# Kernel tuning notes

Hardware: AMD Instinct MI355X
Metric: run time of the kernel (lower is better)

The kernel has to match this reference:

```python
import jax, jax.numpy as jnp
import numpy as np

TOP_K = 2
NEG_INF = -1.0e9


def setup_inputs() -> dict:
    key = jax.random.key(0)
    k = jax.random.split(key, 5)
    B, S, D, E = 4, 2048, 1024, 8
    H = 2 * D
    x = jax.random.normal(k[0], (B, S, D), dtype=jnp.float32)
    gate_w = jax.random.normal(k[1], (D, E), dtype=jnp.float32) * 0.02
    gate_b = jnp.zeros((E,), dtype=jnp.float32)
    w1 = jax.random.normal(k[2], (E, D, H), dtype=jnp.float32) * 0.02
    b1 = jnp.zeros((E, H), dtype=jnp.float32)
    w2 = jax.random.normal(k[3], (E, H, D), dtype=jnp.float32) * 0.02
    b2 = jnp.zeros((E, D), dtype=jnp.float32)
    noise = jax.random.normal(k[4], (B, S, E), dtype=jnp.float32)
    return {"x": x, "gate_w": gate_w, "gate_b": gate_b,
            "w1": w1, "b1": b1, "w2": w2, "b2": b2, "noise": noise}


def reference(x, gate_w, gate_b, w1, b1, w2, b2, noise):
    B, S, D = x.shape
    # Gating: linear + small gaussian noise (hk.next_rng_key equivalent)
    gating_logits = jnp.einsum('bsd,de->bse', x, gate_w) + gate_b + noise * 0.01
    # keep_top_k: mask all but top-k logits to -1e9
    top_k_values, top_k_indices = jax.lax.top_k(gating_logits, TOP_K)
    mask = gating_logits >= jnp.min(top_k_values, axis=-1, keepdims=True)
    gating_logits = jnp.where(mask, gating_logits, NEG_INF)
    gating_probs = jax.nn.softmax(gating_logits, axis=-1)
    # Dense compute of ALL experts on ALL tokens (as in source): [E,B,S,D]
    h = jax.nn.silu(jnp.einsum('bsd,edh->ebsh', x, w1) + b1[:, None, None, :])
    expert_outputs = jnp.einsum('ebsh,ehd->ebsd', h, w2) + b2[:, None, None, :]
    # Gather top-k expert outputs per token: [B,S,K,D]
    bi = jnp.arange(B)[:, None, None]
    si = jnp.arange(S)[None, :, None]
    selected = expert_outputs[top_k_indices, bi, si]
    top_k_gating_probs = jnp.take_along_axis(gating_probs, top_k_indices, axis=-1)
    final_output = jnp.einsum('bskd,bsk->bsd', selected, top_k_gating_probs)
    # Load-balancing aux loss on the MASKED logits (as in source)
    routing_probs = jax.nn.softmax(gating_logits, axis=-1)
    expert_usage = jnp.sum(routing_probs, axis=(0, 1))
    expert_importance = expert_usage / jnp.sum(expert_usage)
    mean_imp = jnp.mean(expert_importance)
    std_imp = jnp.std(expert_importance)
    aux_loss = std_imp / (mean_imp + 1e-10)
    return final_output, top_k_indices, aux_loss
```

## Files before the change

### kernel.cpp

```cpp
#include <hip/hip_runtime.h>
#include <stdint.h>


#define NTOK   8192
#define DIM    1024
#define NEXP   8
#define HID    2048
#define OUT_MAIN (NTOK * DIM)
#define IDX_OFF  OUT_MAIN
#define AUX_OFF  (OUT_MAIN + NTOK * 2)
#define MAXBLK 72

typedef __attribute__((ext_vector_type(8))) short short8;
typedef __attribute__((ext_vector_type(4))) float floatx4;

__device__ __forceinline__ unsigned short f2bf(float f) {
  unsigned int b = __float_as_uint(f);
  b += 0x7FFFu + ((b >> 16) & 1u);
  return (unsigned short)(b >> 16);
}

__global__ __launch_bounds__(1024) void k_gating(
    const float* __restrict__ x, const float* __restrict__ gate_w,
    const float* __restrict__ gate_b, const float* __restrict__ noise,
    float* __restrict__ out, int* __restrict__ counts,
    int* __restrict__ lists_tok, float* __restrict__ lists_p,
    float* __restrict__ probs_all, unsigned short* __restrict__ xb)
{
  const int lane = threadIdx.x & 63;
  const int wv   = threadIdx.x >> 6;
  const int t    = blockIdx.x * 16 + wv;
  const float* xr = x + (size_t)t * DIM;

  __shared__ int   cnt[NEXP];
  __shared__ int   base[NEXP];
  __shared__ int   s_e[32];
  __shared__ int   s_pos[32];
  __shared__ float s_p[32];
  if (threadIdx.x < NEXP) cnt[threadIdx.x] = 0;

  double acc[NEXP] = {0,0,0,0,0,0,0,0};
  #pragma unroll
  for (int jj = 0; jj < 4; ++jj) {
    const int d0 = lane * 4 + jj * 256;
    const float4 xv = *(const float4*)(xr + d0);
    const float xs[4] = {xv.x, xv.y, xv.z, xv.w};
    unsigned short xbq[4];
    #pragma unroll
    for (int c = 0; c < 4; ++c) {
      const float4 g0 = *(const float4*)(gate_w + (size_t)(d0 + c) * NEXP);
      const float4 g1 = *(const float4*)(gate_w + (size_t)(d0 + c) * NEXP + 4);
      const double xd = (double)xs[c];
      acc[0] += xd * (double)g0.x; acc[1] += xd * (double)g0.y;
      acc[2] += xd * (double)g0.z; acc[3] += xd * (double)g0.w;
      acc[4] += xd * (double)g1.x; acc[5] += xd * (double)g1.y;
      acc[6] += xd * (double)g1.z; acc[7] += xd * (double)g1.w;
      xbq[c] = f2bf(xs[c]);
    }
    ushort4 q; q.x = xbq[0]; q.y = xbq[1]; q.z = xbq[2]; q.w = xbq[3];
    *(ushort4*)(xb + (size_t)t * DIM + d0) = q;
  }
  #pragma unroll
  for (int e = 0; e < NEXP; ++e) {
    #pragma unroll
    for (int off = 32; off; off >>= 1) acc[e] += __shfl_xor(acc[e], off);
  }
  __syncthreads();
  if (lane == 0) {
    double l[NEXP];
    #pragma unroll
    for (int e = 0; e < NEXP; ++e)
      l[e] = acc[e] + (double)gate_b[e] + 0.01 * (double)noise[(size_t)t * NEXP + e];
    int i1 = 0; double v1 = l[0];
    #pragma unroll
    for (int e = 1; e < NEXP; ++e) if (l[e] > v1) { v1 = l[e]; i1 = e; }
    int i2 = (i1 == 0) ? 1 : 0; double v2 = l[i2];
    #pragma unroll
    for (int e = 0; e < NEXP; ++e) if (e != i1 && l[e] > v2) { v2 = l[e]; i2 = e; }
    float pr[NEXP]; float Z = 0.f;
    #pragma unroll
    for (int e = 0; e < NEXP; ++e) {
      const float a = (l[e] >= v2) ? (float)(l[e] - v1) : -1.0e9f;
      pr[e] = __expf(a); Z += pr[e];
    }
    const float rz = 1.0f / Z;
    #pragma unroll
    for (int e = 0; e < NEXP; ++e) {
      pr[e] *= rz;
      probs_all[(size_t)t * NEXP + e] = pr[e];
    }
    out[(size_t)IDX_OFF + t * 2]     = (float)i1;
    out[(size_t)IDX_OFF + t * 2 + 1] = (float)i2;
    const int p1 = atomicAdd(&cnt[i1], 1);
    const int p2 = atomicAdd(&cnt[i2], 1);
    s_e[wv * 2]     = i1; s_pos[wv * 2]     = p1; s_p[wv * 2]     = pr[i1];
    s_e[wv * 2 + 1] = i2; s_pos[wv * 2 + 1] = p2; s_p[wv * 2 + 1] = pr[i2];
  }
  __syncthreads();
  if (threadIdx.x < NEXP) base[threadIdx.x] = atomicAdd(&counts[threadIdx.x], cnt[threadIdx.x]);
  __syncthreads();
  if (lane == 0) {
    #pragma unroll
    for (int k = 0; k < 2; ++k) {
      const int ee  = s_e[wv * 2 + k];
      const int pos = base[ee] + s_pos[wv * 2 + k];
      lists_tok[ee * NTOK + pos] = t;
      lists_p[ee * NTOK + pos]   = s_p[wv * 2 + k];
    }
  }
}

__global__ void k_offs(const int* __restrict__ counts, int* __restrict__ offs,
                       int* __restrict__ tbl_e, int* __restrict__ tbl_m,
                       int* __restrict__ nblk) {
  if (threadIdx.x == 0) {
    int a = 0;
    #pragma unroll
    for (int e = 0; e < NEXP; ++e) { offs[e] = a; a += counts[e]; }
    offs[NEXP] = a;
    int ent_e[MAXBLK], ent_m[MAXBLK];
    int nb = 0;
    for (int e = 0; e < NEXP; ++e) {
      const int nbe = (counts[e] + 255) >> 8;
      for (int m = 0; m < nbe; ++m) { ent_e[nb] = e; ent_m[nb] = m << 8; ++nb; }
    }
    nblk[0] = nb;
    for (int p = 0; p < MAXBLK; ++p) { tbl_e[p] = -1; tbl_m[p] = 0; }
    const int q = nb >> 3, r = nb & 7;
    for (int c = 0; c < 8; ++c) {
      const int cnt   = q + (c < r ? 1 : 0);
      const int start = c * q + (c < r ? c : r);
      for (int t = 0; t < cnt; ++t) {
        const int pos = c + (t << 3);
        tbl_e[pos] = ent_e[start + t];
        tbl_m[pos] = ent_m[start + t];
      }
    }
  }
}

__global__ __launch_bounds__(256) void k_aux(const float* __restrict__ probs_all,
                                             float* __restrict__ out) {
  float p[NEXP] = {0,0,0,0,0,0,0,0};
  for (int t = threadIdx.x; t < NTOK; t += 256) {
    const float4 a = *(const float4*)(probs_all + (size_t)t * NEXP);
    const float4 b = *(const float4*)(probs_all + (size_t)t * NEXP + 4);
    p[0] += a.x; p[1] += a.y; p[2] += a.z; p[3] += a.w;
    p[4] += b.x; p[5] += b.y; p[6] += b.z; p[7] += b.w;
  }
  #pragma unroll
  for (int e = 0; e < NEXP; ++e) {
    #pragma unroll
    for (int off = 32; off; off >>= 1) p[e] += __shfl_xor(p[e], off);
  }
  __shared__ float red[4][NEXP];
  const int lane = threadIdx.x & 63, wv = threadIdx.x >> 6;
  if (lane == 0) {
    #pragma unroll
    for (int e = 0; e < NEXP; ++e) red[wv][e] = p[e];
  }
  __syncthreads();
  if (threadIdx.x == 0) {
    float usage[NEXP], s = 0.f;
    #pragma unroll
    for (int e = 0; e < NEXP; ++e) {
      usage[e] = red[0][e] + red[1][e] + red[2][e] + red[3][e];
      s += usage[e];
    }
    float imp[NEXP], mean = 0.f, var = 0.f;
    #pragma unroll
    for (int e = 0; e < NEXP; ++e) { imp[e] = usage[e] / s; mean += imp[e]; }
    mean *= 0.125f;
    #pragma unroll
    for (int e = 0; e < NEXP; ++e) { const float d = imp[e] - mean; var += d * d; }
    var *= 0.125f;
    out[AUX_OFF] = sqrtf(var) / (mean + 1e-10f);
  }
}

__global__ __launch_bounds__(256) void k_tr(
    const float* __restrict__ in, unsigned short* __restrict__ out,
    int in_ld, size_t in_estride, int r0, int c0,
    int out_ld, size_t out_estride)
{
  const int e  = blockIdx.z;
  const int tr = blockIdx.x << 6;
  const int tc = blockIdx.y << 6;
  const int tid = threadIdx.x;
  __shared__ float t[64][65];
  const float* src = in + (size_t)e * in_estride + (size_t)(r0 + tr) * in_ld + (c0 + tc);
  #pragma unroll
  for (int p = 0; p < 4; ++p) {
    const int r  = (p << 4) + (tid >> 4);
    const int c4 = (tid & 15) << 2;
    const float4 v = *(const float4*)(src + (size_t)r * in_ld + c4);
    t[r][c4] = v.x; t[r][c4 + 1] = v.y; t[r][c4 + 2] = v.z; t[r][c4 + 3] = v.w;
  }
  __syncthreads();
  unsigned short* dst = out + (size_t)e * out_estride + (size_t)tc * out_ld + tr;
  #pragma unroll
  for (int p = 0; p < 4; ++p) {
    const int c  = (p << 4) + (tid >> 4);
    const int r4 = (tid & 15) << 2;
    ushort4 q;
    q.x = f2bf(t[r4][c]);     q.y = f2bf(t[r4 + 1][c]);
    q.z = f2bf(t[r4 + 2][c]); q.w = f2bf(t[r4 + 3][c]);
    *(ushort4*)(dst + (size_t)c * out_ld + r4) = q;
  }
}

template <int MODE>
__global__ __launch_bounds__(512, 2) void k_gemm(
    const unsigned short* __restrict__ Abase,
    const unsigned short* __restrict__ Bt,
    const float* __restrict__ bias,
    const int* __restrict__ counts, const int* __restrict__ offs,
    const int* __restrict__ tbl_e, const int* __restrict__ tbl_m,
    const int* __restrict__ nblk,
    const int* __restrict__ lists_tok, const float* __restrict__ lists_p,
    unsigned short* __restrict__ hout, float* __restrict__ out,
    const int hb, const int Hs)
{
  const int bx = blockIdx.x;
  const int e  = tbl_e[bx];
  if (e < 0) return;
  const int m0  = tbl_m[bx];
  const int n_e = counts[e];
  const int nb  = blockIdx.y << 8;

  const int Kloc = (MODE == 0) ? DIM : Hs;
  const int nt   = Kloc >> 6;

  const int tid  = threadIdx.x;
  const int lane = tid & 63;
  const int wv   = tid >> 6;
  const int wm   = (wv & 1) << 7;
  const int wn   = (wv >> 1) << 6;

  __shared__ __align__(16) unsigned short as[2][256 * 64];
  __shared__ __align__(16) unsigned short bs[2][256 * 64];
  unsigned short* const A0 = &as[0][0]; unsigned short* const A1 = &as[1][0];
  unsigned short* const B0 = &bs[0][0]; unsigned short* const B1 = &bs[1][0];

  const unsigned short* Bexp = Bt + (size_t)e * ((size_t)DIM * Hs) + (size_t)nb * Kloc;

  const int off_sh = ((lane & 7) ^ (lane >> 3)) << 3;
  const int r0  = (wv << 3) + (lane >> 3);
  const int rb0 = ((wv >> 2) << 6) + ((wv & 3) << 3) + (lane >> 3);
  const unsigned short* pA0; const unsigned short* pA1;
  const unsigned short* pA2; const unsigned short* pA3;
  {
    const unsigned short* p[4];
    #pragma unroll
    for (int qq = 0; qq < 4; ++qq) {
      const int rr = m0 + r0 + (qq << 6);
      const int rc = (rr < n_e) ? rr : (n_e - 1);
      size_t arow;
      if (MODE == 0) arow = (size_t)lists_tok[e * NTOK + rc] * DIM;
      else           arow = (size_t)(offs[e] + rc) * Hs;
      p[qq] = Abase + arow + off_sh;
    }
    pA0 = p[0]; pA1 = p[1]; pA2 = p[2]; pA3 = p[3];
  }
  const unsigned short* pB0 = Bexp + (size_t)rb0 * Kloc + off_sh;
  const unsigned short* pB1 = Bexp + (size_t)(rb0 + 32) * Kloc + off_sh;
  const unsigned short* pB2 = Bexp + (size_t)(rb0 + 128) * Kloc + off_sh;
  const unsigned short* pB3 = Bexp + (size_t)(rb0 + 160) * Kloc + off_sh;
  const int dA = (wv << 3) * 64;
  const int dB = (((wv >> 2) << 6) + ((wv & 3) << 3)) * 64;

  auto ST = [&](const unsigned short* g, unsigned short* l) {
    __builtin_amdgcn_global_load_lds(
        (const __attribute__((address_space(1))) void*)g,
        (__attribute__((address_space(3))) void*)(void*)l, 16, 0, 0);
  };
  auto STG_A0 = [&](unsigned short* ab, int t) { if (t < nt) { const int kk = t << 6;
      ST(pA0 + kk, ab + dA); ST(pA2 + kk, ab + 2 * 4096 + dA); } };
  auto STG_A1 = [&](unsigned short* ab, int t) { if (t < nt) { const int kk = t << 6;
      ST(pA1 + kk, ab + 4096 + dA); ST(pA3 + kk, ab + 3 * 4096 + dA); } };
  auto STG_B0 = [&](unsigned short* bb, int t) { if (t < nt) { const int kk = t << 6;
      ST(pB0 + kk, bb + dB); ST(pB2 + kk, bb + 8192 + dB); } };
  auto STG_B1 = [&](unsigned short* bb, int t) { if (t < nt) { const int kk = t << 6;
      ST(pB1 + kk, bb + 2048 + dB); ST(pB3 + kk, bb + 10240 + dB); } };

  auto LDA8 = [&](const unsigned short* ab, int i, int s) -> short8 {
    const int row = wm + (i << 4) + (lane & 15);
    const int ck  = (((s << 2) | (lane >> 4)) ^ (row & 7)) << 3;
    return *(const short8*)(ab + row * 64 + ck);
  };
  auto LDB8 = [&](const unsigned short* bb, int j, int s) -> short8 {
    const int row = wn + (j << 4) + (lane & 15);
    const int ck  = (((s << 2) | (lane >> 4)) ^ (row & 7)) << 3;
    return *(const short8*)(bb + row * 64 + ck);
  };

  floatx4 acc[8][4];
  #pragma unroll
  for (int i = 0; i < 8; ++i)
    #pragma unroll
    for (int j = 0; j < 4; ++j) acc[i][j] = (floatx4){0.f, 0.f, 0.f, 0.f};

  STG_A0(A0, 0); STG_B1(B0, 0); STG_A1(A0, 0); STG_B0(B0, 0);
  STG_A0(A1, 1); STG_B1(B1, 1); STG_A1(A1, 1);

  short8 a_[4][2], b_[2][2];
  for (int u = 0; u < nt; ++u) {
    const int p = u & 1;
    const unsigned short* ap = p ? A1 : A0;
    const unsigned short* bp = p ? B1 : B0;
    unsigned short* apn = p ? A0 : A1;
    unsigned short* apc = p ? A1 : A0;
    unsigned short* bpn = p ? B0 : B1;
    unsigned short* bpc = p ? B1 : B0;
    (void)apn;

    STG_B0(bpn, u + 1);
    if (u + 1 < nt) { asm volatile("s_waitcnt vmcnt(8)" ::: "memory"); }
    else            { asm volatile("s_waitcnt vmcnt(0)" ::: "memory"); }
    __builtin_amdgcn_sched_barrier(0);
    __builtin_amdgcn_s_barrier();
    __builtin_amdgcn_sched_barrier(0);
    #pragma unroll
    for (int i = 0; i < 4; ++i) { a_[i][0] = LDA8(ap, i, 0); a_[i][1] = LDA8(ap, i, 1); }
    #pragma unroll
    for (int j = 0; j < 2; ++j) { b_[j][0] = LDB8(bp, j, 0); b_[j][1] = LDB8(bp, j, 1); }
    asm volatile("s_waitcnt lgkmcnt(0)" ::: "memory");
    __builtin_amdgcn_sched_barrier(0);
    __builtin_amdgcn_s_setprio(1);
    #pragma unroll
    for (int s = 0; s < 2; ++s)
      #pragma unroll
      for (int i = 0; i < 4; ++i)
        #pragma unroll
        for (int j = 0; j < 2; ++j)
          acc[i][j] = __builtin_amdgcn_mfma_f32_16x16x32_bf16(a_[i][s], b_[j][s], acc[i][j], 0, 0, 0);
    __builtin_amdgcn_s_setprio(0);
    __builtin_amdgcn_sched_barrier(0);
    __builtin_amdgcn_s_barrier();
    __builtin_amdgcn_sched_barrier(0);

    STG_A0(apc, u + 2);
    #pragma unroll
    for (int j = 0; j < 2; ++j) { b_[j][0] = LDB8(bp, j + 2, 0); b_[j][1] = LDB8(bp, j + 2, 1); }
    __builtin_amdgcn_sched_barrier(0);
    __builtin_amdgcn_s_barrier();
    __builtin_amdgcn_sched_barrier(0);
    asm volatile("s_waitcnt lgkmcnt(0)" ::: "memory");
    __builtin_amdgcn_sched_barrier(0);
    __builtin_amdgcn_s_setprio(1);
    #pragma unroll
    for (int s = 0; s < 2; ++s)
      #pragma unroll
      for (int i = 0; i < 4; ++i)
        #pragma unroll
        for (int j = 0; j < 2; ++j)
          acc[i][j + 2] = __builtin_amdgcn_mfma_f32_16x16x32_bf16(a_[i][s], b_[j][s], acc[i][j + 2], 0, 0, 0);
    __builtin_amdgcn_s_setprio(0);
    __builtin_amdgcn_sched_barrier(0);
    __builtin_amdgcn_s_barrier();
    __builtin_amdgcn_sched_barrier(0);

    STG_B1(bpc, u + 2);
    #pragma unroll
    for (int i = 0; i < 4; ++i) { a_[i][0] = LDA8(ap, i + 4, 0); a_[i][1] = LDA8(ap, i + 4, 1); }
    __builtin_amdgcn_sched_barrier(0);
    __builtin_amdgcn_s_barrier();
    __builtin_amdgcn_sched_barrier(0);
    asm volatile("s_waitcnt lgkmcnt(0)" ::: "memory");
    __builtin_amdgcn_sched_barrier(0);
    __builtin_amdgcn_s_setprio(1);
    #pragma unroll
    for (int s = 0; s < 2; ++s)
      #pragma unroll
      for (int i = 0; i < 4; ++i)
        #pragma unroll
        for (int j = 0; j < 2; ++j)
          acc[i + 4][j + 2] = __builtin_amdgcn_mfma_f32_16x16x32_bf16(a_[i][s], b_[j][s], acc[i + 4][j + 2], 0, 0, 0);
    __builtin_amdgcn_s_setprio(0);
    __builtin_amdgcn_sched_barrier(0);
    __builtin_amdgcn_s_barrier();
    __builtin_amdgcn_sched_barrier(0);

    STG_A1(apc, u + 2);
    #pragma unroll
    for (int j = 0; j < 2; ++j) { b_[j][0] = LDB8(bp, j, 0); b_[j][1] = LDB8(bp, j, 1); }
    __builtin_amdgcn_sched_barrier(0);
    __builtin_amdgcn_s_barrier();
    __builtin_amdgcn_sched_barrier(0);
    asm volatile("s_waitcnt lgkmcnt(0)" ::: "memory");
    __builtin_amdgcn_sched_barrier(0);
    __builtin_amdgcn_s_setprio(1);
    #pragma unroll
    for (int s = 0; s < 2; ++s)
      #pragma unroll
      for (int i = 0; i < 4; ++i)
        #pragma unroll
        for (int j = 0; j < 2; ++j)
          acc[i + 4][j] = __builtin_amdgcn_mfma_f32_16x16x32_bf16(a_[i][s], b_[j][s], acc[i + 4][j], 0, 0, 0);
    __builtin_amdgcn_s_setprio(0);
    __builtin_amdgcn_sched_barrier(0);
    __builtin_amdgcn_s_barrier();
    __builtin_amdgcn_sched_barrier(0);
  }

  const int q4 = (lane >> 4) << 2;
  if (MODE == 0) {
    #pragma unroll
    for (int i = 0; i < 8; ++i) {
      #pragma unroll
      for (int j = 0; j < 4; ++j) {
        const int nloc = wn + (j << 4) + (lane & 15);
        const float bb = bias[e * HID + hb + nb + nloc];
        #pragma unroll
        for (int rr = 0; rr < 4; ++rr) {
          const int m = m0 + wm + (i << 4) + q4 + rr;
          if (m < n_e) {
            float v = acc[i][j][rr] + bb;
            v = v / (1.0f + __expf(-v));
            hout[(size_t)(offs[e] + m) * Hs + nb + nloc] = f2bf(v);
          }
        }
      }
    }
  } else {
    #pragma unroll
    for (int i = 0; i < 8; ++i) {
      #pragma unroll
      for (int rr = 0; rr < 4; ++rr) {
        const int m = m0 + wm + (i << 4) + q4 + rr;
        if (m < n_e) {
          const int   tok = lists_tok[e * NTOK + m];
          const float pp  = lists_p[e * NTOK + m];
          #pragma unroll
          for (int j = 0; j < 4; ++j) {
            const int d = nb + wn + (j << 4) + (lane & 15);
            float v = acc[i][j][rr];
            if (hb == 0) v += bias[e * DIM + d];
            atomicAdd(out + (size_t)tok * DIM + d, pp * v);
          }
        }
      }
    }
  }
}

extern "C" void kernel_launch(void* const* d_in, const int* in_sizes, int n_in,
                              void* d_out, int out_size, void* d_ws, size_t ws_size,
                              hipStream_t stream)
{
  const float* x      = (const float*)d_in[0];
  const float* gate_w = (const float*)d_in[1];
  const float* gate_b = (const float*)d_in[2];
  const float* w1     = (const float*)d_in[3];
  const float* b1     = (const float*)d_in[4];
  const float* w2     = (const float*)d_in[5];
  const float* b2     = (const float*)d_in[6];
  const float* noise  = (const float*)d_in[7];
  float* out = (float*)d_out;

  char* ws = (char*)d_ws;
  const size_t CNT_OFF = 0;
  const size_t OFF_OFF = 64;
  const size_t NBK_OFF = 128;
  const size_t TBE_OFF = 192;
  const size_t TBM_OFF = 1024;
  const size_t LT_OFF  = 2048;
  const size_t LP_OFF  = LT_OFF + 262144;
  const size_t PA_OFF  = LP_OFF + 262144;
  const size_t XB_OFF  = 1048576;
  const size_t W_OFF   = 17825792;

  int nsl = 0;
  for (int cand = 1; cand <= 8; cand <<= 1) {
    const size_t need = W_OFF + (size_t)(33554432 + 67108864) / (size_t)cand;
    if (ws_size >= need) { nsl = cand; break; }
  }
  if (!nsl) return;
  const int Hs = HID / nsl;

  int* counts          = (int*)(ws + CNT_OFF);
  int* offs            = (int*)(ws + OFF_OFF);
  int* nblk            = (int*)(ws + NBK_OFF);
  int* tbl_e           = (int*)(ws + TBE_OFF);
  int* tbl_m           = (int*)(ws + TBM_OFF);
  int* lists_tok       = (int*)(ws + LT_OFF);
  float* lists_p       = (float*)(ws + LP_OFF);
  float* probs_all     = (float*)(ws + PA_OFF);
  unsigned short* xb   = (unsigned short*)(ws + XB_OFF);
  unsigned short* wt   = (unsigned short*)(ws + W_OFF);
  unsigned short* hbuf = (unsigned short*)(ws + W_OFF + (size_t)33554432 / nsl);

  hipMemsetAsync(d_out, 0, (size_t)OUT_MAIN * sizeof(float), stream);
  hipMemsetAsync(ws + CNT_OFF, 0, 64, stream);

  k_gating<<<NTOK / 16, 1024, 0, stream>>>(x, gate_w, gate_b, noise, out, counts,
                                           lists_tok, lists_p, probs_all, xb);
  k_offs<<<1, 64, 0, stream>>>(counts, offs, tbl_e, tbl_m, nblk);
  k_aux<<<1, 256, 0, stream>>>(probs_all, out);

  for (int s = 0; s < nsl; ++s) {
    const int hb = s * Hs;
    dim3 gt1(DIM / 64, Hs / 64, NEXP);
    k_tr<<<gt1, 256, 0, stream>>>(w1, wt, HID, (size_t)DIM * HID, 0, hb,
                                  DIM, (size_t)Hs * DIM);
    dim3 g1(MAXBLK, Hs / 256, 1);
    k_gemm<0><<<g1, 512, 0, stream>>>(xb, wt, b1, counts, offs, tbl_e, tbl_m, nblk,
                                      lists_tok, lists_p, hbuf, out, hb, Hs);
    dim3 gt2(Hs / 64, DIM / 64, NEXP);
    k_tr<<<gt2, 256, 0, stream>>>(w2, wt, DIM, (size_t)DIM * HID, hb, 0,
                                  Hs, (size_t)DIM * Hs);
    dim3 g2(MAXBLK, DIM / 256, 1);
    k_gemm<1><<<g2, 512, 0, stream>>>(hbuf, wt, b2, counts, offs, tbl_e, tbl_m, nblk,
                                      lists_tok, lists_p, hbuf, out, hb, Hs);
  }
}
```

Measured before the change: 496.4 us.

## Split-K the second expert GEMM and reorder the MFMA pipeline stages

The down-projection GEMM gets a split-K over two halves of the hidden dimension, which doubles its grid so more CUs are occupied, and the partial sums are combined through the atomicAdd epilogue that already exists. The bias is added only by the first K-half. The main loop is also reorganised: A fragments are reused across B halves in a different quadrant order, the explicit lgkmcnt waits between phases are removed, and the vmcnt threshold changes. In exchange the output gets twice as many atomic adds, and dropping the LDS waits leans on the compiler to insert them correctly.

```diff
diff --git a/kernel.cpp b/kernel.cpp
--- a/kernel.cpp
+++ b/kernel.cpp
@@ -226,10 +226,12 @@
   if (e < 0) return;
   const int m0  = tbl_m[bx];
   const int n_e = counts[e];
-  const int nb  = blockIdx.y << 8;
-
-  const int Kloc = (MODE == 0) ? DIM : Hs;
-  const int nt   = Kloc >> 6;
+  const int by  = blockIdx.y;
+
+  int nb, k0g, Kloc;
+  if (MODE == 0) { nb = by << 8; k0g = 0; Kloc = DIM; }
+  else { nb = (by >> 1) << 8; const int half = Hs >> 1;
+         k0g = (by & 1) * half; Kloc = half; }
 
   const int tid  = threadIdx.x;
   const int lane = tid & 63;
@@ -242,56 +244,58 @@
   unsigned short* const A0 = &as[0][0]; unsigned short* const A1 = &as[1][0];
   unsigned short* const B0 = &bs[0][0]; unsigned short* const B1 = &bs[1][0];
 
-  const unsigned short* Bexp = Bt + (size_t)e * ((size_t)DIM * Hs) + (size_t)nb * Kloc;
+  const int K = (MODE == 0) ? DIM : Hs;
+  const unsigned short* Bexp = Bt + (size_t)e * ((size_t)DIM * Hs) + (size_t)nb * K + k0g;
 
   const int off_sh = ((lane & 7) ^ (lane >> 3)) << 3;
-  const int r0  = (wv << 3) + (lane >> 3);
-  const int rb0 = ((wv >> 2) << 6) + ((wv & 3) << 3) + (lane >> 3);
+  const int rw = (wv << 3) + (lane >> 3);
   const unsigned short* pA0; const unsigned short* pA1;
   const unsigned short* pA2; const unsigned short* pA3;
   {
     const unsigned short* p[4];
     #pragma unroll
-    for (int qq = 0; qq < 4; ++qq) {
-      const int rr = m0 + r0 + (qq << 6);
+    for (int q = 0; q < 4; ++q) {
+      const int rr = m0 + rw + (q << 6);
       const int rc = (rr < n_e) ? rr : (n_e - 1);
       size_t arow;
       if (MODE == 0) arow = (size_t)lists_tok[e * NTOK + rc] * DIM;
       else           arow = (size_t)(offs[e] + rc) * Hs;
-      p[qq] = Abase + arow + off_sh;
+      p[q] = Abase + arow + k0g + off_sh;
     }
     pA0 = p[0]; pA1 = p[1]; pA2 = p[2]; pA3 = p[3];
   }
-  const unsigned short* pB0 = Bexp + (size_t)rb0 * Kloc + off_sh;
-  const unsigned short* pB1 = Bexp + (size_t)(rb0 + 32) * Kloc + off_sh;
-  const unsigned short* pB2 = Bexp + (size_t)(rb0 + 128) * Kloc + off_sh;
-  const unsigned short* pB3 = Bexp + (size_t)(rb0 + 160) * Kloc + off_sh;
-  const int dA = (wv << 3) * 64;
-  const int dB = (((wv >> 2) << 6) + ((wv & 3) << 3)) * 64;
+  const int rB1 = (rw & 31) + ((rw >> 5) << 6);
+  const unsigned short* pBl0 = Bexp + (size_t)rB1 * K + off_sh;
+  const unsigned short* pBl1 = Bexp + (size_t)(rB1 + 128) * K + off_sh;
+  const unsigned short* pBh0 = Bexp + (size_t)(rB1 + 32) * K + off_sh;
+  const unsigned short* pBh1 = Bexp + (size_t)(rB1 + 160) * K + off_sh;
+  const int dA0 = (wv << 3) * 64;
+  const int RBw = ((wv << 3) & 31) + (((wv << 3) >> 5) << 6);
+  const int dB0 = RBw * 64;
 
   auto ST = [&](const unsigned short* g, unsigned short* l) {
     __builtin_amdgcn_global_load_lds(
         (const __attribute__((address_space(1))) void*)g,
         (__attribute__((address_space(3))) void*)(void*)l, 16, 0, 0);
   };
-  auto STG_A0 = [&](unsigned short* ab, int t) { if (t < nt) { const int kk = t << 6;
-      ST(pA0 + kk, ab + dA); ST(pA2 + kk, ab + 2 * 4096 + dA); } };
-  auto STG_A1 = [&](unsigned short* ab, int t) { if (t < nt) { const int kk = t << 6;
-      ST(pA1 + kk, ab + 4096 + dA); ST(pA3 + kk, ab + 3 * 4096 + dA); } };
-  auto STG_B0 = [&](unsigned short* bb, int t) { if (t < nt) { const int kk = t << 6;
-      ST(pB0 + kk, bb + dB); ST(pB2 + kk, bb + 8192 + dB); } };
-  auto STG_B1 = [&](unsigned short* bb, int t) { if (t < nt) { const int kk = t << 6;
-      ST(pB1 + kk, bb + 2048 + dB); ST(pB3 + kk, bb + 10240 + dB); } };
-
+  const int nt = Kloc >> 6;
+  auto STG_Alo = [&](unsigned short* ab, int t) { if (t < nt) { const int kk = t << 6;
+      ST(pA0 + kk, ab + dA0); ST(pA2 + kk, ab + 128 * 64 + dA0); } };
+  auto STG_Ahi = [&](unsigned short* ab, int t) { if (t < nt) { const int kk = t << 6;
+      ST(pA1 + kk, ab + 64 * 64 + dA0); ST(pA3 + kk, ab + 192 * 64 + dA0); } };
+  auto STG_Blo = [&](unsigned short* bb, int t) { if (t < nt) { const int kk = t << 6;
+      ST(pBl0 + kk, bb + dB0); ST(pBl1 + kk, bb + 128 * 64 + dB0); } };
+  auto STG_Bhi = [&](unsigned short* bb, int t) { if (t < nt) { const int kk = t << 6;
+      ST(pBh0 + kk, bb + 32 * 64 + dB0); ST(pBh1 + kk, bb + 160 * 64 + dB0); } };
+
+  const int c = lane >> 4;
   auto LDA8 = [&](const unsigned short* ab, int i, int s) -> short8 {
     const int row = wm + (i << 4) + (lane & 15);
-    const int ck  = (((s << 2) | (lane >> 4)) ^ (row & 7)) << 3;
-    return *(const short8*)(ab + row * 64 + ck);
+    return *(const short8*)(ab + row * 64 + ((((s << 2) | c) ^ (row & 7)) << 3));
   };
   auto LDB8 = [&](const unsigned short* bb, int j, int s) -> short8 {
     const int row = wn + (j << 4) + (lane & 15);
-    const int ck  = (((s << 2) | (lane >> 4)) ^ (row & 7)) << 3;
-    return *(const short8*)(bb + row * 64 + ck);
+    return *(const short8*)(bb + row * 64 + ((((s << 2) | c) ^ (row & 7)) << 3));
   };
 
   floatx4 acc[8][4];
@@ -300,32 +304,48 @@
     #pragma unroll
     for (int j = 0; j < 4; ++j) acc[i][j] = (floatx4){0.f, 0.f, 0.f, 0.f};
 
-  STG_A0(A0, 0); STG_B1(B0, 0); STG_A1(A0, 0); STG_B0(B0, 0);
-  STG_A0(A1, 1); STG_B1(B1, 1); STG_A1(A1, 1);
-
-  short8 a_[4][2], b_[2][2];
+  STG_Alo(A0, 0); STG_Blo(B0, 0); STG_Ahi(A0, 0); STG_Bhi(B0, 0);
+  STG_Blo(B1, 1); STG_Ahi(A1, 1); STG_Bhi(B1, 1);
+
   for (int u = 0; u < nt; ++u) {
-    const int p = u & 1;
-    const unsigned short* ap = p ? A1 : A0;
-    const unsigned short* bp = p ? B1 : B0;
-    unsigned short* apn = p ? A0 : A1;
-    unsigned short* apc = p ? A1 : A0;
-    unsigned short* bpn = p ? B0 : B1;
-    unsigned short* bpc = p ? B1 : B0;
-    (void)apn;
-
-    STG_B0(bpn, u + 1);
-    if (u + 1 < nt) { asm volatile("s_waitcnt vmcnt(8)" ::: "memory"); }
+    const int pb = u & 1;
+    const unsigned short* ap = pb ? A1 : A0;
+    const unsigned short* bp = pb ? B1 : B0;
+    unsigned short* aN = pb ? A0 : A1;
+    unsigned short* aC = pb ? A1 : A0;
+    unsigned short* bC = pb ? B1 : B0;
+
+    short8 bk[2][2], ah[4][2], bh[2][2];
+
+    if (u + 1 < nt) { asm volatile("s_waitcnt vmcnt(6)" ::: "memory"); }
     else            { asm volatile("s_waitcnt vmcnt(0)" ::: "memory"); }
     __builtin_amdgcn_sched_barrier(0);
     __builtin_amdgcn_s_barrier();
     __builtin_amdgcn_sched_barrier(0);
-    #pragma unroll
-    for (int i = 0; i < 4; ++i) { a_[i][0] = LDA8(ap, i, 0); a_[i][1] = LDA8(ap, i, 1); }
-    #pragma unroll
-    for (int j = 0; j < 2; ++j) { b_[j][0] = LDB8(bp, j, 0); b_[j][1] = LDB8(bp, j, 1); }
-    asm volatile("s_waitcnt lgkmcnt(0)" ::: "memory");
-    __builtin_amdgcn_sched_barrier(0);
+    STG_Alo(aN, u + 1);
+    {
+      short8 al[4][2];
+      #pragma unroll
+      for (int i = 0; i < 4; ++i) { al[i][0] = LDA8(ap, i, 0); al[i][1] = LDA8(ap, i, 1); }
+      #pragma unroll
+      for (int j = 0; j < 2; ++j) { bk[j][0] = LDB8(bp, j, 0); bk[j][1] = LDB8(bp, j, 1); }
+      __builtin_amdgcn_s_setprio(1);
+      #pragma unroll
+      for (int s = 0; s < 2; ++s)
+        #pragma unroll
+        for (int i = 0; i < 4; ++i)
+          #pragma unroll
+          for (int j = 0; j < 2; ++j)
+            acc[i][j] = __builtin_amdgcn_mfma_f32_16x16x32_bf16(al[i][s], bk[j][s], acc[i][j], 0, 0, 0);
+      __builtin_amdgcn_s_setprio(0);
+    }
+    __builtin_amdgcn_sched_barrier(0);
+    __builtin_amdgcn_s_barrier();
+    __builtin_amdgcn_sched_barrier(0);
+
+    STG_Blo(bC, u + 2);
+    #pragma unroll
+    for (int i = 0; i < 4; ++i) { ah[i][0] = LDA8(ap, i + 4, 0); ah[i][1] = LDA8(ap, i + 4, 1); }
     __builtin_amdgcn_s_setprio(1);
     #pragma unroll
     for (int s = 0; s < 2; ++s)
@@ -333,20 +353,15 @@
       for (int i = 0; i < 4; ++i)
         #pragma unroll
         for (int j = 0; j < 2; ++j)
-          acc[i][j] = __builtin_amdgcn_mfma_f32_16x16x32_bf16(a_[i][s], b_[j][s], acc[i][j], 0, 0, 0);
+          acc[i + 4][j] = __builtin_amdgcn_mfma_f32_16x16x32_bf16(ah[i][s], bk[j][s], acc[i + 4][j], 0, 0, 0);
     __builtin_amdgcn_s_setprio(0);
     __builtin_amdgcn_sched_barrier(0);
     __builtin_amdgcn_s_barrier();
     __builtin_amdgcn_sched_barrier(0);
 
-    STG_A0(apc, u + 2);
-    #pragma unroll
-    for (int j = 0; j < 2; ++j) { b_[j][0] = LDB8(bp, j + 2, 0); b_[j][1] = LDB8(bp, j + 2, 1); }
-    __builtin_amdgcn_sched_barrier(0);
-    __builtin_amdgcn_s_barrier();
-    __builtin_amdgcn_sched_barrier(0);
-    asm volatile("s_waitcnt lgkmcnt(0)" ::: "memory");
-    __builtin_amdgcn_sched_barrier(0);
+    STG_Ahi(aC, u + 2);
+    #pragma unroll
+    for (int j = 0; j < 2; ++j) { bh[j][0] = LDB8(bp, j + 2, 0); bh[j][1] = LDB8(bp, j + 2, 1); }
     __builtin_amdgcn_s_setprio(1);
     #pragma unroll
     for (int s = 0; s < 2; ++s)
@@ -354,50 +369,27 @@
       for (int i = 0; i < 4; ++i)
         #pragma unroll
         for (int j = 0; j < 2; ++j)
-          acc[i][j + 2] = __builtin_amdgcn_mfma_f32_16x16x32_bf16(a_[i][s], b_[j][s], acc[i][j + 2], 0, 0, 0);
+          acc[i + 4][j + 2] = __builtin_amdgcn_mfma_f32_16x16x32_bf16(ah[i][s], bh[j][s], acc[i + 4][j + 2], 0, 0, 0);
     __builtin_amdgcn_s_setprio(0);
     __builtin_amdgcn_sched_barrier(0);
     __builtin_amdgcn_s_barrier();
     __builtin_amdgcn_sched_barrier(0);
 
-    STG_B1(bpc, u + 2);
-    #pragma unroll
-    for (int i = 0; i < 4; ++i) { a_[i][0] = LDA8(ap, i + 4, 0); a_[i][1] = LDA8(ap, i + 4, 1); }
-    __builtin_amdgcn_sched_barrier(0);
-    __builtin_amdgcn_s_barrier();
-    __builtin_amdgcn_sched_barrier(0);
-    asm volatile("s_waitcnt lgkmcnt(0)" ::: "memory");
-    __builtin_amdgcn_sched_barrier(0);
-    __builtin_amdgcn_s_setprio(1);
-    #pragma unroll
-    for (int s = 0; s < 2; ++s)
-      #pragma unroll
-      for (int i = 0; i < 4; ++i)
+    STG_Bhi(bC, u + 2);
+    {
+      short8 al[4][2];
+      #pragma unroll
+      for (int i = 0; i < 4; ++i) { al[i][0] = LDA8(ap, i, 0); al[i][1] = LDA8(ap, i, 1); }
+      __builtin_amdgcn_s_setprio(1);
+      #pragma unroll
+      for (int s = 0; s < 2; ++s)
         #pragma unroll
-        for (int j = 0; j < 2; ++j)
-          acc[i + 4][j + 2] = __builtin_amdgcn_mfma_f32_16x16x32_bf16(a_[i][s], b_[j][s], acc[i + 4][j + 2], 0, 0, 0);
-    __builtin_amdgcn_s_setprio(0);
-    __builtin_amdgcn_sched_barrier(0);
-    __builtin_amdgcn_s_barrier();
-    __builtin_amdgcn_sched_barrier(0);
-
-    STG_A1(apc, u + 2);
-    #pragma unroll
-    for (int j = 0; j < 2; ++j) { b_[j][0] = LDB8(bp, j, 0); b_[j][1] = LDB8(bp, j, 1); }
-    __builtin_amdgcn_sched_barrier(0);
-    __builtin_amdgcn_s_barrier();
-    __builtin_amdgcn_sched_barrier(0);
-    asm volatile("s_waitcnt lgkmcnt(0)" ::: "memory");
-    __builtin_amdgcn_sched_barrier(0);
-    __builtin_amdgcn_s_setprio(1);
-    #pragma unroll
-    for (int s = 0; s < 2; ++s)
-      #pragma unroll
-      for (int i = 0; i < 4; ++i)
-        #pragma unroll
-        for (int j = 0; j < 2; ++j)
-          acc[i + 4][j] = __builtin_amdgcn_mfma_f32_16x16x32_bf16(a_[i][s], b_[j][s], acc[i + 4][j], 0, 0, 0);
-    __builtin_amdgcn_s_setprio(0);
+        for (int i = 0; i < 4; ++i)
+          #pragma unroll
+          for (int j = 0; j < 2; ++j)
+            acc[i][j + 2] = __builtin_amdgcn_mfma_f32_16x16x32_bf16(al[i][s], bh[j][s], acc[i][j + 2], 0, 0, 0);
+      __builtin_amdgcn_s_setprio(0);
+    }
     __builtin_amdgcn_sched_barrier(0);
     __builtin_amdgcn_s_barrier();
     __builtin_amdgcn_sched_barrier(0);
@@ -435,7 +427,7 @@
           for (int j = 0; j < 4; ++j) {
             const int d = nb + wn + (j << 4) + (lane & 15);
             float v = acc[i][j][rr];
-            if (hb == 0) v += bias[e * DIM + d];
+            if (hb == 0 && k0g == 0) v += bias[e * DIM + d];
             atomicAdd(out + (size_t)tok * DIM + d, pp * v);
           }
         }
@@ -509,7 +501,7 @@
     dim3 gt2(Hs / 64, DIM / 64, NEXP);
     k_tr<<<gt2, 256, 0, stream>>>(w2, wt, DIM, (size_t)DIM * HID, hb, 0,
                                   Hs, (size_t)DIM * Hs);
-    dim3 g2(MAXBLK, DIM / 256, 1);
+    dim3 g2(MAXBLK, (DIM / 256) * 2, 1);
     k_gemm<1><<<g2, 512, 0, stream>>>(hbuf, wt, b2, counts, offs, tbl_e, tbl_m, nblk,
                                       lists_tok, lists_p, hbuf, out, hb, Hs);
   }
```

Measured after the change: 467.3 us. 1.06x faster.
